# Kernel tuning notes

Hardware: AMD Instinct MI355X
Metric: run time of the kernel (lower is better)

Reference implementation:

```python
import jax, jax.numpy as jnp
import numpy as np

N, E, F, H, B = 100000, 600000, 128, 128, 250


def setup_inputs() -> dict:
    key = jax.random.key(0)
    ks = jax.random.split(key, 10)
    x = jax.random.normal(ks[0], (N, F), dtype=jnp.float32)
    # last two columns encode cluster id c in {0,1,2}: c = x[:,-1] + 2*x[:,-2]
    c = jax.random.randint(ks[1], (N,), 0, 3)
    x = x.at[:, -2].set((c == 2).astype(jnp.float32))
    x = x.at[:, -1].set((c == 1).astype(jnp.float32))
    edge_index = jax.random.randint(ks[2], (2, E), 0, N, dtype=jnp.int64)
    batch = (jnp.arange(N, dtype=jnp.int64) // (N // B))  # 400 nodes per graph
    s = 1.0 / np.sqrt(F)
    sh = 1.0 / np.sqrt(H)
    W1 = jax.random.uniform(ks[3], (F, H), jnp.float32, -s, s)
    b1 = jnp.zeros((H,), jnp.float32)
    W2 = jax.random.uniform(ks[4], (H, H), jnp.float32, -sh, sh)
    b2 = jnp.zeros((H,), jnp.float32)
    W3 = jax.random.uniform(ks[5], (H, H), jnp.float32, -sh, sh)
    b3 = jnp.zeros((H,), jnp.float32)
    sl = 1.0 / np.sqrt(3 * H)
    Wl = jax.random.uniform(ks[6], (3 * H, 1), jnp.float32, -sl, sl)
    bl = jax.random.uniform(ks[7], (1,), jnp.float32, -sl, sl)
    return {"x": x, "edge_index": edge_index, "batch": batch,
            "W1": W1, "b1": b1, "W2": W2, "b2": b2, "W3": W3, "b3": b3,
            "Wl": Wl, "bl": bl}


def _gcn_conv(h, W, b, src, dst, dinv):
    # PyG GCNConv: h @ W, then D^{-1/2} (A + I) D^{-1/2} aggregation, + bias.
    h = h @ W
    norm = dinv[src] * dinv[dst]              # [E+N]
    msg = h[src] * norm[:, None]              # gather + scale
    out = jax.ops.segment_sum(msg, dst, num_segments=N)  # scatter-add at target
    return out + b


def _forward(x, edge_index, batch, W1, b1, W2, b2, W3, b3, Wl, bl):
    cluster = (x[:, -1] + 2.0 * x[:, -2]).astype(jnp.int64)  # in {0,1,2}
    loop = jnp.arange(N, dtype=edge_index.dtype)
    src = jnp.concatenate([edge_index[0], loop])  # self-loops appended
    dst = jnp.concatenate([edge_index[1], loop])
    deg = jax.ops.segment_sum(jnp.ones_like(dst, dtype=x.dtype), dst, num_segments=N)
    dinv = jax.lax.rsqrt(jnp.maximum(deg, 1.0))  # deg >= 1 via self-loops

    h = jax.nn.relu(_gcn_conv(x, W1, b1, src, dst, dinv))
    h = jax.nn.relu(_gcn_conv(h, W2, b2, src, dst, dinv))
    h = _gcn_conv(h, W3, b3, src, dst, dinv)

    cb = batch * 3 + cluster                   # segment id per (graph, cluster)
    sums = jax.ops.segment_sum(h, cb, num_segments=B * 3)
    cnts = jax.ops.segment_sum(jnp.ones((N,), h.dtype), cb, num_segments=B * 3)
    xc = sums / jnp.maximum(cnts, 1.0)[:, None]  # scatter-mean
    z = xc.reshape(B, 3 * H)                   # dropout p=0.2 is identity in eval
    return jax.nn.sigmoid(z @ Wl + bl)


def reference(x, edge_index, batch, W1, b1, W2, b2, W3, b3, Wl, bl):
    return _forward(x, edge_index, batch, W1, b1, W2, b2, W3, b3, Wl, bl)
```

## Files before the change

### kernel.cpp

```cpp
#include <hip/hip_runtime.h>
#include <hip/hip_bf16.h>
#include <math.h>


#define WAVE 64
#define NPARTS 25
#define WPAD 136
#define ELLK 32

typedef __attribute__((ext_vector_type(8))) short bf16x8;
typedef __attribute__((ext_vector_type(4))) float f32x4;
typedef __attribute__((ext_vector_type(2))) float f32x2;

__device__ __forceinline__ unsigned short bf16r(float f) {
    unsigned u = __float_as_uint(f);
    return (unsigned short)((u + 0x7fffu + ((u >> 16) & 1u)) >> 16);
}
__device__ __forceinline__ unsigned pack_bf16(float a, float b) {
    return (unsigned)bf16r(a) | ((unsigned)bf16r(b) << 16);
}
__device__ __forceinline__ unsigned pack_fp8x4(float a, float b, float c, float d) {
    unsigned u = (unsigned)__builtin_amdgcn_cvt_pk_fp8_f32(a, b, 0, false);
    u = (unsigned)__builtin_amdgcn_cvt_pk_fp8_f32(c, d, (int)u, true);
    return u;
}
__device__ __forceinline__ void fma8_fp8(float* acc, float w, uint2 u) {
    f32x2 p0 = __builtin_amdgcn_cvt_pk_f32_fp8((int)u.x, false);
    f32x2 p1 = __builtin_amdgcn_cvt_pk_f32_fp8((int)u.x, true);
    f32x2 p2 = __builtin_amdgcn_cvt_pk_f32_fp8((int)u.y, false);
    f32x2 p3 = __builtin_amdgcn_cvt_pk_f32_fp8((int)u.y, true);
    acc[0] += w * p0.x; acc[1] += w * p0.y;
    acc[2] += w * p1.x; acc[3] += w * p1.y;
    acc[4] += w * p2.x; acc[5] += w * p2.y;
    acc[6] += w * p3.x; acc[7] += w * p3.y;
}

__device__ __forceinline__ void agg_node(const uint2* __restrict__ hb2,
                                         const int* __restrict__ deg,
                                         const int* __restrict__ ce,
                                         int nc, bool ok, int sl, float* acc) {
    uint2 self = hb2[(size_t)nc * 16 + sl];
    for (int j = 0; j < 8; ++j) acc[j] = 0.f;
    fma8_fp8(acc, 1.f, self);
    int dg = ok ? min(deg[nc], ELLK) : 0;
    const int base = nc * ELLK;
    int c0, c1, c2, c3;
    if (dg > 0) {
        int dm = dg - 1;
        c0 = ce[base];
        c1 = ce[base + min(1, dm)];
        c2 = ce[base + min(2, dm)];
        c3 = ce[base + min(3, dm)];
    }
    for (int i = 0; i < dg; i += 4) {
        int p0 = c0, p1 = c1, p2 = c2, p3 = c3;
        int nx = i + 4;
        if (nx < dg) {
            int dm = dg - 1;
            c0 = ce[base + nx];
            c1 = ce[base + min(nx + 1, dm)];
            c2 = ce[base + min(nx + 2, dm)];
            c3 = ce[base + min(nx + 3, dm)];
        }
        uint2 u0 = hb2[(size_t)p0 * 16 + sl];
        uint2 u1 = hb2[(size_t)p1 * 16 + sl];
        uint2 u2 = hb2[(size_t)p2 * 16 + sl];
        uint2 u3 = hb2[(size_t)p3 * 16 + sl];
        float w1 = (i + 1 < dg) ? 1.f : 0.f;
        float w2 = (i + 2 < dg) ? 1.f : 0.f;
        float w3 = (i + 3 < dg) ? 1.f : 0.f;
        fma8_fp8(acc, 1.f, u0);
        fma8_fp8(acc, w1, u1);
        fma8_fp8(acc, w2, u2);
        fma8_fp8(acc, w3, u3);
    }
}


__global__ void fill_ell(const int* __restrict__ src, const int* __restrict__ dst,
                         int* __restrict__ deg, int* __restrict__ ce, int ne,
                         const float* __restrict__ W1, const float* __restrict__ W2,
                         const float* __restrict__ W3, const float* __restrict__ Wl,
                         unsigned short* __restrict__ Wt, float* __restrict__ wv,
                         int fb) {
    int b = blockIdx.x;
    int t = threadIdx.x;
    if (b < fb) {
        int e = b * 256 + t;
        if (e < ne) {
            int d = dst[e], s = src[e];
            int slot = atomicAdd(&deg[d], 1);
            if (slot < ELLK) ce[d * ELLK + slot] = s;
        }
        return;
    }
    int p = b - fb;
    if (p < 128) {
        int idx = (p & 63) * 256 + t;
        int layer = p >> 6;
        const float* W = (layer == 0) ? W1 : W2;
        int n = idx >> 7, k = idx & 127;
        Wt[layer * 16384 + n * 128 + k] = bf16r(W[k * 128 + n]);
    } else {
        int idx = (p - 128) * 256 + t;
        if (idx < 384) {
            int c = idx >> 7, k = idx & 127;
            const float* wlc = Wl + c * 128;
            const float* w3r = W3 + k * 128;
            float s = 0.f;
#pragma unroll 8
            for (int n = 0; n < 128; ++n) s += w3r[n] * wlc[n];
            wv[c * 128 + k] = s;
        }
    }
}


__global__ void prep_kernel(const float* __restrict__ x, unsigned* __restrict__ hb,
                            const int* __restrict__ deg, float* __restrict__ dinv,
                            int* __restrict__ cluster, int n32) {
    int i = blockIdx.x * blockDim.x + threadIdx.x;
    if (i >= n32) return;
    int row = i >> 5;
    float di = rsqrtf((float)(deg[row] + 1));
    float4 v = ((const float4*)x)[i];
    hb[i] = pack_fp8x4(di * v.x, di * v.y, di * v.z, di * v.w);
    if ((i & 31) == 31) {
        dinv[row] = di;
        cluster[row] = (int)(v.w + 2.0f * v.z + 0.5f);
    }
}


__global__ void agg_kernel(const uint2* __restrict__ hb2, uint4* __restrict__ out4,
                           const int* __restrict__ deg, const int* __restrict__ ce,
                           const float* __restrict__ dinv, int n) {
    int wid = blockIdx.x * (blockDim.x >> 6) + (threadIdx.x >> 6);
    int lane = threadIdx.x & 63;
    int g = lane >> 4, sl = lane & 15;
    int node = wid * 4 + g;
    bool ok = node < n;
    int nc = ok ? node : (n - 1);
    float acc[8];
    agg_node(hb2, deg, ce, nc, ok, sl, acc);
    if (ok) {
        float di = dinv[nc];
        uint4 o;
        o.x = pack_bf16(di * acc[0], di * acc[1]);
        o.y = pack_bf16(di * acc[2], di * acc[3]);
        o.z = pack_bf16(di * acc[4], di * acc[5]);
        o.w = pack_bf16(di * acc[6], di * acc[7]);
        out4[(size_t)node * 16 + sl] = o;
    }
}


__global__ __launch_bounds__(256) void agg_pool(
    const uint2* __restrict__ hb2,
    const int* __restrict__ deg, const int* __restrict__ ce,
    const float* __restrict__ dinv, const int* __restrict__ cluster,
    float* __restrict__ psums, int* __restrict__ pcnts, int n) {
    __shared__ float smW[4][3][128];
    __shared__ int smC[4][3];
    const int t = threadIdx.x;
    for (int i = t; i < 4 * 3 * 128; i += 256) ((float*)smW)[i] = 0.f;
    if (t < 12) ((int*)smC)[t] = 0;
    __syncthreads();

    const int wave = t >> 6, lane = t & 63;
    const int g = lane >> 4, sl = lane & 15;
    const int node = blockIdx.x * 16 + wave * 4 + g;
    const bool ok = node < n;
    const int nc = ok ? node : (n - 1);
    float acc[8];
    agg_node(hb2, deg, ce, nc, ok, sl, acc);
    const float di = ok ? dinv[nc] : 0.f;

    const int cl = ok ? cluster[nc] : 0;
#pragma unroll
    for (int g2 = 0; g2 < 4; ++g2) {
        if (g == g2 && ok) {
            float* dstp = &smW[wave][cl][sl * 8];
#pragma unroll
            for (int j = 0; j < 8; ++j) dstp[j] += di * acc[j];
            if (sl == 0) smC[wave][cl] += 1;
        }
    }
    __syncthreads();

    if (t < 128) {
#pragma unroll
        for (int c = 0; c < 3; ++c) {
            float s = smW[0][c][t] + smW[1][c][t] + smW[2][c][t] + smW[3][c][t];
            psums[((size_t)blockIdx.x * 3 + c) * 128 + t] = s;
        }
    }
    if (t < 3)
        pcnts[blockIdx.x * 3 + t] = smC[0][t] + smC[1][t] + smC[2][t] + smC[3][t];
}


__global__ __launch_bounds__(256) void gemm_mfma(const unsigned short* __restrict__ A,
                                                 const unsigned short* __restrict__ Wt,
                                                 const float* __restrict__ bias,
                                                 const float* __restrict__ dinv,
                                                 unsigned char* __restrict__ Cb,
                                                 int n) {
    __shared__ unsigned short sm[128 * WPAD];
    const int t = threadIdx.x;
    const int wave = t >> 6, lane = t & 63;
    const int quad = lane >> 4, lr = lane & 15;
    const size_t row0 = (size_t)blockIdx.x * 128 + wave * 32;

    {
        int r = t >> 1, h = t & 1;
        const uint4* s = (const uint4*)(Wt + r * 128 + h * 64);
        uint4* d = (uint4*)(sm + r * WPAD + h * 64);
#pragma unroll
        for (int i = 0; i < 8; ++i) d[i] = s[i];
    }
    __syncthreads();

    f32x4 acc[2][8];
#pragma unroll
    for (int i2 = 0; i2 < 2; ++i2)
#pragma unroll
        for (int ct = 0; ct < 8; ++ct) acc[i2][ct] = (f32x4){0.f, 0.f, 0.f, 0.f};

    const unsigned short* arow0 = A + (row0 + lr) * 128;
    const unsigned short* arow1 = arow0 + 16 * 128;
#pragma unroll
    for (int kc = 0; kc < 4; ++kc) {
        int kb = kc * 32 + quad * 8;
        bf16x8 a0 = *(const bf16x8*)(arow0 + kb);
        bf16x8 a1 = *(const bf16x8*)(arow1 + kb);
#pragma unroll
        for (int ct = 0; ct < 8; ++ct) {
            bf16x8 w = *(const bf16x8*)(sm + (ct * 16 + lr) * WPAD + kb);
            acc[0][ct] = __builtin_amdgcn_mfma_f32_16x16x32_bf16(w, a0, acc[0][ct], 0, 0, 0);
            acc[1][ct] = __builtin_amdgcn_mfma_f32_16x16x32_bf16(w, a1, acc[1][ct], 0, 0, 0);
        }
    }

#pragma unroll
    for (int i2 = 0; i2 < 2; ++i2) {
        int row = (int)row0 + i2 * 16 + lr;
        float di = (row < n) ? dinv[row] : 0.f;
        unsigned char* crow = Cb + (size_t)row * 128;
#pragma unroll
        for (int ct = 0; ct < 8; ++ct) {
            float4 bq = *(const float4*)&bias[ct * 16 + quad * 4];
            float v0 = di * fmaxf(acc[i2][ct][0] + bq.x, 0.f);
            float v1 = di * fmaxf(acc[i2][ct][1] + bq.y, 0.f);
            float v2 = di * fmaxf(acc[i2][ct][2] + bq.z, 0.f);
            float v3 = di * fmaxf(acc[i2][ct][3] + bq.w, 0.f);
            *(unsigned*)(crow + ct * 16 + quad * 4) = pack_fp8x4(v0, v1, v2, v3);
        }
    }
}

__global__ void head_kernel(const float* __restrict__ part_sums,
                            const int* __restrict__ part_cnts,
                            const float* __restrict__ wv, const float* __restrict__ b3,
                            const float* __restrict__ Wl, const float* __restrict__ bl,
                            float* __restrict__ out) {
    int b = blockIdx.x, t = threadIdx.x;
    float s0 = 0.f, s1 = 0.f, s2 = 0.f;
    int n0 = 0, n1 = 0, n2 = 0;
#pragma unroll
    for (int p = 0; p < NPARTS; ++p) {
        int blk = b * NPARTS + p;
        size_t o = (size_t)blk * 384 + t;
        s0 += part_sums[o];
        s1 += part_sums[o + 128];
        s2 += part_sums[o + 256];
        n0 += part_cnts[blk * 3 + 0];
        n1 += part_cnts[blk * 3 + 1];
        n2 += part_cnts[blk * 3 + 2];
    }
    float bt = b3[t];
    float z = 0.f;
    if (n0 > 0) z += (s0 / (float)n0) * wv[t]       + bt * Wl[t];
    if (n1 > 0) z += (s1 / (float)n1) * wv[128 + t] + bt * Wl[128 + t];
    if (n2 > 0) z += (s2 / (float)n2) * wv[256 + t] + bt * Wl[256 + t];
    for (int off = 32; off > 0; off >>= 1) z += __shfl_down(z, off);
    __shared__ float partial[2];
    if ((t & 63) == 0) partial[t >> 6] = z;
    __syncthreads();
    if (t == 0) {
        float zz = partial[0] + partial[1] + bl[0];
        out[b] = 1.0f / (1.0f + expf(-zz));
    }
}


extern "C" void kernel_launch(void* const* d_in, const int* in_sizes, int n_in,
                              void* d_out, int out_size, void* d_ws, size_t ws_size,
                              hipStream_t stream) {
    const float* x  = (const float*)d_in[0];
    const int*   ei = (const int*)d_in[1];
    const float* W1 = (const float*)d_in[3];
    const float* b1 = (const float*)d_in[4];
    const float* W2 = (const float*)d_in[5];
    const float* b2 = (const float*)d_in[6];
    const float* W3 = (const float*)d_in[7];
    const float* b3 = (const float*)d_in[8];
    const float* Wl = (const float*)d_in[9];
    const float* bl = (const float*)d_in[10];
    float* out = (float*)d_out;

    const int N = in_sizes[0] / 128;
    const int E = in_sizes[1] / 2;
    const int B = out_size;
    const int Npad = (N + 127) & ~127;

    const int* srcp = ei;
    const int* dstp = ei + E;

    char* ws = (char*)d_ws;
    size_t off = 0;
    auto alloc = [&](size_t bytes) -> char* {
        char* p = ws + off;
        off += (bytes + 255) & ~(size_t)255;
        return p;
    };
    unsigned char*  hb = (unsigned char*) alloc((size_t)Npad * 128);
    unsigned short* ab = (unsigned short*)alloc((size_t)Npad * 128 * 2);
    unsigned short* wt = (unsigned short*)alloc((size_t)2 * 16384 * 2);
    float* wv      = (float*)alloc(384 * 4);
    float* dinv    = (float*)alloc((size_t)N * 4);
    int*   cluster = (int*)  alloc((size_t)N * 4);
    int*   ce      = (int*)  alloc((size_t)N * ELLK * 4);
    float* psums   = (float*)alloc((size_t)B * NPARTS * 3 * 128 * 4);
    int*   pcnts   = (int*)  alloc((size_t)B * NPARTS * 3 * 4);
    int*   deg     = (int*)  alloc((size_t)N * 4);
    (void)ws_size; (void)n_in;

    hipMemsetAsync(deg, 0, (size_t)N * 4, stream);

    int fb = (E + 255) / 256;
    fill_ell<<<fb + 130, 256, 0, stream>>>(srcp, dstp, deg, ce, E,
                                           W1, W2, W3, Wl, wt, wv, fb);
    prep_kernel<<<(N * 32 + 255) / 256, 256, 0, stream>>>(x, (unsigned*)hb, deg,
                                                          dinv, cluster, N * 32);

    int gemmBlocks = Npad / 128;
    int aggBlocks = (N + 15) / 16;

    agg_kernel<<<aggBlocks, 256, 0, stream>>>((const uint2*)hb, (uint4*)ab,
                                              deg, ce, dinv, N);
    gemm_mfma<<<gemmBlocks, 256, 0, stream>>>(ab, wt,         b1, dinv, hb, N);
    agg_kernel<<<aggBlocks, 256, 0, stream>>>((const uint2*)hb, (uint4*)ab,
                                              deg, ce, dinv, N);
    gemm_mfma<<<gemmBlocks, 256, 0, stream>>>(ab, wt + 16384, b2, dinv, hb, N);

    agg_pool<<<aggBlocks, 256, 0, stream>>>((const uint2*)hb, deg, ce,
                                            dinv, cluster, psums, pcnts, N);
    head_kernel<<<B, 128, 0, stream>>>(psums, pcnts, wv, b3, Wl, bl, out);
}
```

Baseline: 252.8 us.

## Switch GEMM operands and aggregation output to FP8 and unroll gather by eight

The aggregation output and the transposed weights are now stored as FP8 instead of BF16, and the GEMM uses the fp8×fp8 16x16x32 MFMA with a smaller shared-memory weight tile. This halves the bytes written by the aggregation and read by the GEMM, and halves the weight staging traffic. The neighbor gather loop now prefetches and processes 8 neighbors per iteration instead of 4, which raises memory-level parallelism but uses more registers and wastes more masked loads on low-degree nodes. FP8 operands reduce accuracy in both GCN layers.

```diff
diff --git a/kernel.cpp b/kernel.cpp
--- a/kernel.cpp
+++ b/kernel.cpp
@@ -5,19 +5,15 @@
 
 #define WAVE 64
 #define NPARTS 25
-#define WPAD 136
+#define WPADB 144
 #define ELLK 32
 
-typedef __attribute__((ext_vector_type(8))) short bf16x8;
 typedef __attribute__((ext_vector_type(4))) float f32x4;
 typedef __attribute__((ext_vector_type(2))) float f32x2;
 
 __device__ __forceinline__ unsigned short bf16r(float f) {
     unsigned u = __float_as_uint(f);
     return (unsigned short)((u + 0x7fffu + ((u >> 16) & 1u)) >> 16);
-}
-__device__ __forceinline__ unsigned pack_bf16(float a, float b) {
-    return (unsigned)bf16r(a) | ((unsigned)bf16r(b) << 16);
 }
 __device__ __forceinline__ unsigned pack_fp8x4(float a, float b, float c, float d) {
     unsigned u = (unsigned)__builtin_amdgcn_cvt_pk_fp8_f32(a, b, 0, false);
@@ -44,35 +40,56 @@
     fma8_fp8(acc, 1.f, self);
     int dg = ok ? min(deg[nc], ELLK) : 0;
     const int base = nc * ELLK;
-    int c0, c1, c2, c3;
+    int c0, c1, c2, c3, c4, c5, c6, c7;
     if (dg > 0) {
         int dm = dg - 1;
         c0 = ce[base];
         c1 = ce[base + min(1, dm)];
         c2 = ce[base + min(2, dm)];
         c3 = ce[base + min(3, dm)];
-    }
-    for (int i = 0; i < dg; i += 4) {
+        c4 = ce[base + min(4, dm)];
+        c5 = ce[base + min(5, dm)];
+        c6 = ce[base + min(6, dm)];
+        c7 = ce[base + min(7, dm)];
+    }
+    for (int i = 0; i < dg; i += 8) {
         int p0 = c0, p1 = c1, p2 = c2, p3 = c3;
-        int nx = i + 4;
+        int p4 = c4, p5 = c5, p6 = c6, p7 = c7;
+        int nx = i + 8;
         if (nx < dg) {
             int dm = dg - 1;
             c0 = ce[base + nx];
             c1 = ce[base + min(nx + 1, dm)];
             c2 = ce[base + min(nx + 2, dm)];
             c3 = ce[base + min(nx + 3, dm)];
+            c4 = ce[base + min(nx + 4, dm)];
+            c5 = ce[base + min(nx + 5, dm)];
+            c6 = ce[base + min(nx + 6, dm)];
+            c7 = ce[base + min(nx + 7, dm)];
         }
         uint2 u0 = hb2[(size_t)p0 * 16 + sl];
         uint2 u1 = hb2[(size_t)p1 * 16 + sl];
         uint2 u2 = hb2[(size_t)p2 * 16 + sl];
         uint2 u3 = hb2[(size_t)p3 * 16 + sl];
+        uint2 u4 = hb2[(size_t)p4 * 16 + sl];
+        uint2 u5 = hb2[(size_t)p5 * 16 + sl];
+        uint2 u6 = hb2[(size_t)p6 * 16 + sl];
+        uint2 u7 = hb2[(size_t)p7 * 16 + sl];
         float w1 = (i + 1 < dg) ? 1.f : 0.f;
         float w2 = (i + 2 < dg) ? 1.f : 0.f;
         float w3 = (i + 3 < dg) ? 1.f : 0.f;
+        float w4 = (i + 4 < dg) ? 1.f : 0.f;
+        float w5 = (i + 5 < dg) ? 1.f : 0.f;
+        float w6 = (i + 6 < dg) ? 1.f : 0.f;
+        float w7 = (i + 7 < dg) ? 1.f : 0.f;
         fma8_fp8(acc, 1.f, u0);
         fma8_fp8(acc, w1, u1);
         fma8_fp8(acc, w2, u2);
         fma8_fp8(acc, w3, u3);
+        fma8_fp8(acc, w4, u4);
+        fma8_fp8(acc, w5, u5);
+        fma8_fp8(acc, w6, u6);
+        fma8_fp8(acc, w7, u7);
     }
 }
 
@@ -81,7 +98,7 @@
                          int* __restrict__ deg, int* __restrict__ ce, int ne,
                          const float* __restrict__ W1, const float* __restrict__ W2,
                          const float* __restrict__ W3, const float* __restrict__ Wl,
-                         unsigned short* __restrict__ Wt, float* __restrict__ wv,
+                         unsigned* __restrict__ Wt, float* __restrict__ wv,
                          int fb) {
     int b = blockIdx.x;
     int t = threadIdx.x;
@@ -95,14 +112,18 @@
         return;
     }
     int p = b - fb;
-    if (p < 128) {
-        int idx = (p & 63) * 256 + t;
-        int layer = p >> 6;
+    if (p < 32) {
+        int layer = p >> 4;
+        int idx = (p & 15) * 256 + t;
         const float* W = (layer == 0) ? W1 : W2;
-        int n = idx >> 7, k = idx & 127;
-        Wt[layer * 16384 + n * 128 + k] = bf16r(W[k * 128 + n]);
+        int n = idx >> 5, k4 = (idx & 31) * 4;
+        float a = W[(k4 + 0) * 128 + n];
+        float bb = W[(k4 + 1) * 128 + n];
+        float c = W[(k4 + 2) * 128 + n];
+        float d = W[(k4 + 3) * 128 + n];
+        Wt[layer * 4096 + n * 32 + (idx & 31)] = pack_fp8x4(a, bb, c, d);
     } else {
-        int idx = (p - 128) * 256 + t;
+        int idx = (p - 32) * 256 + t;
         if (idx < 384) {
             int c = idx >> 7, k = idx & 127;
             const float* wlc = Wl + c * 128;
@@ -132,7 +153,7 @@
 }
 
 
-__global__ void agg_kernel(const uint2* __restrict__ hb2, uint4* __restrict__ out4,
+__global__ void agg_kernel(const uint2* __restrict__ hb2, uint2* __restrict__ out2,
                            const int* __restrict__ deg, const int* __restrict__ ce,
                            const float* __restrict__ dinv, int n) {
     int wid = blockIdx.x * (blockDim.x >> 6) + (threadIdx.x >> 6);
@@ -145,12 +166,10 @@
     agg_node(hb2, deg, ce, nc, ok, sl, acc);
     if (ok) {
         float di = dinv[nc];
-        uint4 o;
-        o.x = pack_bf16(di * acc[0], di * acc[1]);
-        o.y = pack_bf16(di * acc[2], di * acc[3]);
-        o.z = pack_bf16(di * acc[4], di * acc[5]);
-        o.w = pack_bf16(di * acc[6], di * acc[7]);
-        out4[(size_t)node * 16 + sl] = o;
+        uint2 o;
+        o.x = pack_fp8x4(di * acc[0], di * acc[1], di * acc[2], di * acc[3]);
+        o.y = pack_fp8x4(di * acc[4], di * acc[5], di * acc[6], di * acc[7]);
+        out2[(size_t)node * 16 + sl] = o;
     }
 }
 
@@ -200,13 +219,13 @@
 }
 
 
-__global__ __launch_bounds__(256) void gemm_mfma(const unsigned short* __restrict__ A,
-                                                 const unsigned short* __restrict__ Wt,
+__global__ __launch_bounds__(256) void gemm_mfma(const unsigned char* __restrict__ A,
+                                                 const unsigned char* __restrict__ Wt,
                                                  const float* __restrict__ bias,
                                                  const float* __restrict__ dinv,
                                                  unsigned char* __restrict__ Cb,
                                                  int n) {
-    __shared__ unsigned short sm[128 * WPAD];
+    __shared__ unsigned char sm[128 * WPADB];
     const int t = threadIdx.x;
     const int wave = t >> 6, lane = t & 63;
     const int quad = lane >> 4, lr = lane & 15;
@@ -215,9 +234,9 @@
     {
         int r = t >> 1, h = t & 1;
         const uint4* s = (const uint4*)(Wt + r * 128 + h * 64);
-        uint4* d = (uint4*)(sm + r * WPAD + h * 64);
-#pragma unroll
-        for (int i = 0; i < 8; ++i) d[i] = s[i];
+        uint4* d = (uint4*)(sm + r * WPADB + h * 64);
+#pragma unroll
+        for (int i = 0; i < 4; ++i) d[i] = s[i];
     }
     __syncthreads();
 
@@ -227,18 +246,18 @@
 #pragma unroll
         for (int ct = 0; ct < 8; ++ct) acc[i2][ct] = (f32x4){0.f, 0.f, 0.f, 0.f};
 
-    const unsigned short* arow0 = A + (row0 + lr) * 128;
-    const unsigned short* arow1 = arow0 + 16 * 128;
+    const unsigned char* arow0 = A + (row0 + lr) * 128;
+    const unsigned char* arow1 = arow0 + 16 * 128;
 #pragma unroll
     for (int kc = 0; kc < 4; ++kc) {
         int kb = kc * 32 + quad * 8;
-        bf16x8 a0 = *(const bf16x8*)(arow0 + kb);
-        bf16x8 a1 = *(const bf16x8*)(arow1 + kb);
+        long a0 = *(const long*)(arow0 + kb);
+        long a1 = *(const long*)(arow1 + kb);
 #pragma unroll
         for (int ct = 0; ct < 8; ++ct) {
-            bf16x8 w = *(const bf16x8*)(sm + (ct * 16 + lr) * WPAD + kb);
-            acc[0][ct] = __builtin_amdgcn_mfma_f32_16x16x32_bf16(w, a0, acc[0][ct], 0, 0, 0);
-            acc[1][ct] = __builtin_amdgcn_mfma_f32_16x16x32_bf16(w, a1, acc[1][ct], 0, 0, 0);
+            long w = *(const long*)(sm + (ct * 16 + lr) * WPADB + kb);
+            acc[0][ct] = __builtin_amdgcn_mfma_f32_16x16x32_fp8_fp8(w, a0, acc[0][ct], 0, 0, 0);
+            acc[1][ct] = __builtin_amdgcn_mfma_f32_16x16x32_fp8_fp8(w, a1, acc[1][ct], 0, 0, 0);
         }
     }
 
@@ -325,8 +344,8 @@
         return p;
     };
     unsigned char*  hb = (unsigned char*) alloc((size_t)Npad * 128);
-    unsigned short* ab = (unsigned short*)alloc((size_t)Npad * 128 * 2);
-    unsigned short* wt = (unsigned short*)alloc((size_t)2 * 16384 * 2);
+    unsigned char*  ab = (unsigned char*) alloc((size_t)Npad * 128);
+    unsigned*       wt = (unsigned*)      alloc((size_t)2 * 4096 * 4);
     float* wv      = (float*)alloc(384 * 4);
     float* dinv    = (float*)alloc((size_t)N * 4);
     int*   cluster = (int*)  alloc((size_t)N * 4);
@@ -339,20 +358,22 @@
     hipMemsetAsync(deg, 0, (size_t)N * 4, stream);
 
     int fb = (E + 255) / 256;
-    fill_ell<<<fb + 130, 256, 0, stream>>>(srcp, dstp, deg, ce, E,
-                                           W1, W2, W3, Wl, wt, wv, fb);
+    fill_ell<<<fb + 34, 256, 0, stream>>>(srcp, dstp, deg, ce, E,
+                                          W1, W2, W3, Wl, wt, wv, fb);
     prep_kernel<<<(N * 32 + 255) / 256, 256, 0, stream>>>(x, (unsigned*)hb, deg,
                                                           dinv, cluster, N * 32);
 
     int gemmBlocks = Npad / 128;
     int aggBlocks = (N + 15) / 16;
 
-    agg_kernel<<<aggBlocks, 256, 0, stream>>>((const uint2*)hb, (uint4*)ab,
+    agg_kernel<<<aggBlocks, 256, 0, stream>>>((const uint2*)hb, (uint2*)ab,
                                               deg, ce, dinv, N);
-    gemm_mfma<<<gemmBlocks, 256, 0, stream>>>(ab, wt,         b1, dinv, hb, N);
-    agg_kernel<<<aggBlocks, 256, 0, stream>>>((const uint2*)hb, (uint4*)ab,
+    gemm_mfma<<<gemmBlocks, 256, 0, stream>>>(ab, (const unsigned char*)wt,
+                                              b1, dinv, hb, N);
+    agg_kernel<<<aggBlocks, 256, 0, stream>>>((const uint2*)hb, (uint2*)ab,
                                               deg, ce, dinv, N);
-    gemm_mfma<<<gemmBlocks, 256, 0, stream>>>(ab, wt + 16384, b2, dinv, hb, N);
+    gemm_mfma<<<gemmBlocks, 256, 0, stream>>>(ab, (const unsigned char*)wt + 16384,
+                                              b2, dinv, hb, N);
 
     agg_pool<<<aggBlocks, 256, 0, stream>>>((const uint2*)hb, deg, ce,
                                             dinv, cluster, psums, pcnts, N);
```

After: 249.1 us. No clear change (-1.4%).
